# Performance work log

Hardware: AMD Instinct MI355X
Metric: run time of the kernel (lower is better)

Reference implementation:

```python
import jax, jax.numpy as jnp
from jax import lax
import numpy as np


def _dw_xcorr_single(f, k):
    # f: (ch, Hf, Wf) search features; k: (ch, Hk, Wk) template kernel
    # Depthwise cross-correlation: one 2D correlation per channel.
    ch = f.shape[0]
    out = lax.conv_general_dilated(
        f[None],                 # (1, ch, Hf, Wf)
        k[:, None],              # (ch, 1, Hk, Wk) OIHW depthwise kernel
        window_strides=(1, 1),
        padding='VALID',
        dimension_numbers=('NCHW', 'OIHW', 'NCHW'),
        feature_group_count=ch,
    )
    return out[0]  # (ch, H, W)


def _conv3x3(x, w, b):
    # x: (N, C, H, W), w: (O, C, 3, 3), b: (O,)
    y = lax.conv_general_dilated(
        x, w, window_strides=(1, 1), padding='VALID',
        dimension_numbers=('NCHW', 'OIHW', 'NCHW'))
    return y + b[None, :, None, None]


def setup_inputs() -> dict:
    key = jax.random.key(0)
    k1, k2, k3, k4, k5, k6 = jax.random.split(key, 6)
    N, C = 128, 256
    x_f = jax.random.normal(k1, (N, C, 31, 31), dtype=jnp.float32)
    z_f = jax.random.normal(k2, (N, C, 7, 7), dtype=jnp.float32)
    # Conv params (Kaiming-uniform-like scale)
    s3 = 1.0 / np.sqrt(C * 9)
    heat_w = jax.random.uniform(k3, (1, C, 3, 3), jnp.float32, -s3, s3)
    heat_b = jax.random.uniform(k4, (1,), jnp.float32, -s3, s3)
    reg_w = jax.random.uniform(k5, (4, C, 3, 3), jnp.float32, -s3, s3)
    reg_b = jax.random.uniform(k6, (4,), jnp.float32, -s3, s3)
    return {"x_f": x_f, "z_f": z_f, "heat_w": heat_w, "heat_b": heat_b,
            "reg_w": reg_w, "reg_b": reg_b}


def reference(x_f, z_f, heat_w, heat_b, reg_w, reg_b):
    # Depthwise cross-correlation over batch (groups = N*ch in the original)
    corr = jax.vmap(_dw_xcorr_single)(x_f, z_f)  # (N, C, 25, 25)
    pred_heat = _conv3x3(corr, heat_w, heat_b)   # (N, 1, 23, 23)
    pred_reg = _conv3x3(corr, reg_w, reg_b)      # (N, 4, 23, 23)
    return (pred_heat, pred_reg)
```

## Files before the change

### kernel.cpp

```cpp
#include <hip/hip_runtime.h>

#define NB 128
#define NC 256
#define HX 31
#define WX 31
#define HC 25
#define WC 25
#define HO 23
#define WO 23
#define CHUNKS 16
#define CPB (NC / CHUNKS)
#define GRP 8
#define ZCH 56
#define WCH 48
#define CCH (HC * WC)

#define NPIX (HO * WO)
#define HEAT_SZ (NB * NPIX)
#define REG_SZ  (NB * 4 * NPIX)
#define OUT_TOTAL (HEAT_SZ + REG_SZ)
#define NSTRIP3 (HO * 8)
#define PART_STRIDE (5 * NPIX)
#define WS_NEED ((size_t)NB * CHUNKS * PART_STRIDE * sizeof(float))

typedef float f4v __attribute__((ext_vector_type(4), aligned(4)));

__global__ void init_out_kernel(float* __restrict__ out,
                                const float* __restrict__ heat_b,
                                const float* __restrict__ reg_b) {
    int i = blockIdx.x * 256 + threadIdx.x;
    if (i >= OUT_TOTAL) return;
    if (i < HEAT_SZ) {
        out[i] = heat_b[0];
    } else {
        int j = i - HEAT_SZ;
        int o = (j / NPIX) & 3;
        out[i] = reg_b[o];
    }
}

__global__ void reduce_kernel(const float* __restrict__ part,
                              const float* __restrict__ heat_b,
                              const float* __restrict__ reg_b,
                              float* __restrict__ out) {
    int i = blockIdx.x * 256 + threadIdx.x;
    if (i >= OUT_TOTAL) return;
    int n, o, p;
    float b;
    if (i < HEAT_SZ) {
        n = i / NPIX; p = i - n * NPIX; o = 0; b = heat_b[0];
    } else {
        int j = i - HEAT_SZ;
        n = j / (4 * NPIX);
        int rm = j - n * 4 * NPIX;
        int r = rm / NPIX;
        p = rm - r * NPIX;
        o = 1 + r;
        b = reg_b[r];
    }
    const float* src = part + (size_t)n * CHUNKS * PART_STRIDE + o * NPIX + p;
    float s = b;
    #pragma unroll
    for (int c = 0; c < CHUNKS; ++c) s += src[(size_t)c * PART_STRIDE];
    out[i] = s;
}

template <bool USE_WS>
__launch_bounds__(256, 4)
__global__ void fused_head_kernel(const float* __restrict__ xf,
                                  const float* __restrict__ zf,
                                  const float* __restrict__ hw,
                                  const float* __restrict__ rw,
                                  float* __restrict__ out) {
    __shared__ __align__(16) float cs[GRP * CCH + 8];
    __shared__ __align__(16) float zs[GRP * ZCH];
    __shared__ __align__(16) float ws[CPB * WCH];

    const int tid = threadIdx.x;
    const int n = blockIdx.x >> 4;
    const int chunk = blockIdx.x & 15;
    const int cbase = chunk * CPB;

    const int cl = tid / 25;
    const int tt = tid % 25;
    const int tr = tt / 5, tc = tt % 5;
    const int i0 = tr * 5, j0 = tc * 5;

    const bool hasS = (tid < NSTRIP3);
    const int sy = tid >> 3;
    const int sx = tid & 7;
    const int cx = sx * 3;
    const int offS = sy * WC + cx;

    float accH[3] = {0.f, 0.f, 0.f};
    float accR[4][3] = {{0.f,0.f,0.f},{0.f,0.f,0.f},{0.f,0.f,0.f},{0.f,0.f,0.f}};

    const float* xn = xf + ((size_t)n * NC + cbase) * (HX * WX);
    const float* zn = zf + ((size_t)n * NC + cbase) * 49;

    for (int idx = tid; idx < CPB * 45; idx += 256) {
        int ch = idx / 45, j = idx - ch * 45;
        int c = cbase + ch;
        float v;
        if (j < 9) {
            v = hw[c * 9 + j];
        } else {
            int o = (j - 9) / 9;
            int jj = (j - 9) - o * 9;
            v = rw[((size_t)o * NC + c) * 9 + jj];
        }
        ws[ch * WCH + j] = v;
    }

    for (int g0 = 0; g0 < CPB; g0 += GRP) {
        for (int idx = tid; idx < GRP * 49; idx += 256) {
            int ch = idx / 49, q = idx - ch * 49;
            int u = q / 7, v = q - u * 7;
            zs[ch * ZCH + u * 8 + v] = zn[(size_t)(g0 + ch) * 49 + q];
        }
        __syncthreads();

        if (cl < GRP) {
            const float* xb = xn + (size_t)(g0 + cl) * (HX * WX) + i0 * WX + j0;
            const float* zb = zs + cl * ZCH;

            float cacc[5][5];
            #pragma unroll
            for (int r = 0; r < 5; ++r)
                #pragma unroll
                for (int b = 0; b < 5; ++b) cacc[r][b] = 0.f;

            f4v c0 = *(const f4v*)(xb);
            f4v c1 = *(const f4v*)(xb + 4);
            f4v c2 = *(const f4v*)(xb + 7);

            #pragma unroll
            for (int rl = 0; rl < 11; ++rl) {
                f4v n0, n1, n2;
                if (rl < 10) {
                    const float* rp = xb + (rl + 1) * WX;
                    n0 = *(const f4v*)(rp);
                    n1 = *(const f4v*)(rp + 4);
                    n2 = *(const f4v*)(rp + 7);
                }
                const float xr[11] = {c0.x, c0.y, c0.z, c0.w,
                                      c1.x, c1.y, c1.z, c1.w,
                                      c2.y, c2.z, c2.w};
                #pragma unroll
                for (int u = 0; u < 7; ++u) {
                    const int r = rl - u;
                    if (r >= 0 && r < 5) {
                        f4v za = *(const f4v*)(zb + u * 8);
                        f4v zc = *(const f4v*)(zb + u * 8 + 4);
                        const float zz[7] = {za.x, za.y, za.z, za.w,
                                             zc.x, zc.y, zc.z};
                        #pragma unroll
                        for (int v = 0; v < 7; ++v)
                            #pragma unroll
                            for (int b = 0; b < 5; ++b)
                                cacc[r][b] = fmaf(zz[v], xr[b + v], cacc[r][b]);
                    }
                }
                if (rl < 10) { c0 = n0; c1 = n1; c2 = n2; }
            }
            float* cb = cs + cl * CCH + i0 * WC + j0;
            #pragma unroll
            for (int r = 0; r < 5; ++r)
                #pragma unroll
                for (int b = 0; b < 5; ++b) cb[r * WC + b] = cacc[r][b];
        }
        __syncthreads();

        if (hasS) {
            for (int clc = 0; clc < GRP; ++clc) {
                float w[48];
                {
                    const f4v* wp = (const f4v*)(ws + (size_t)(g0 + clc) * WCH);
                    #pragma unroll
                    for (int q = 0; q < 12; ++q) {
                        f4v t = wp[q];
                        w[q * 4 + 0] = t.x; w[q * 4 + 1] = t.y;
                        w[q * 4 + 2] = t.z; w[q * 4 + 3] = t.w;
                    }
                }
                const float* base = cs + clc * CCH + offS;

                #pragma unroll
                for (int dy = 0; dy < 3; ++dy) {
                    f4v f = *(const f4v*)(base + dy * WC);
                    const float f4 = base[dy * WC + 4];
                    #pragma unroll
                    for (int dx = 0; dx < 3; ++dx) {
                        const int k = dy * 3 + dx;
                        #pragma unroll
                        for (int px = 0; px < 3; ++px) {
                            const int e = dx + px;
                            const float cv = (e < 4) ? f[e] : f4;
                            accH[px]    = fmaf(cv, w[k],      accH[px]);
                            accR[0][px] = fmaf(cv, w[9 + k],  accR[0][px]);
                            accR[1][px] = fmaf(cv, w[18 + k], accR[1][px]);
                            accR[2][px] = fmaf(cv, w[27 + k], accR[2][px]);
                            accR[3][px] = fmaf(cv, w[36 + k], accR[3][px]);
                        }
                    }
                }
            }
        }
        __syncthreads();
    }

    if (!hasS) return;
    const int p = sy * WO + cx;
    const bool full = (sx < 7);

    if (USE_WS) {
        float* part = out + (size_t)(n * CHUNKS + chunk) * PART_STRIDE;
        part[p + 0] = accH[0];
        part[p + 1] = accH[1];
        if (full) part[p + 2] = accH[2];
        #pragma unroll
        for (int o = 0; o < 4; ++o) {
            float* pr = part + (1 + o) * NPIX + p;
            pr[0] = accR[o][0];
            pr[1] = accR[o][1];
            if (full) pr[2] = accR[o][2];
        }
    } else {
        float* outH = out + n * NPIX + p;
        float* outR = out + HEAT_SZ + (size_t)n * 4 * NPIX + p;
        atomicAdd(&outH[0], accH[0]);
        atomicAdd(&outH[1], accH[1]);
        if (full) atomicAdd(&outH[2], accH[2]);
        #pragma unroll
        for (int o = 0; o < 4; ++o) {
            float* pr = outR + o * NPIX;
            atomicAdd(&pr[0], accR[o][0]);
            atomicAdd(&pr[1], accR[o][1]);
            if (full) atomicAdd(&pr[2], accR[o][2]);
        }
    }
}

extern "C" void kernel_launch(void* const* d_in, const int* in_sizes, int n_in,
                              void* d_out, int out_size, void* d_ws, size_t ws_size,
                              hipStream_t stream) {
    const float* x_f    = (const float*)d_in[0];
    const float* z_f    = (const float*)d_in[1];
    const float* heat_w = (const float*)d_in[2];
    const float* heat_b = (const float*)d_in[3];
    const float* reg_w  = (const float*)d_in[4];
    const float* reg_b  = (const float*)d_in[5];
    float* out = (float*)d_out;

    if (d_ws != nullptr && ws_size >= WS_NEED) {
        fused_head_kernel<true><<<NB * CHUNKS, 256, 0, stream>>>(
            x_f, z_f, heat_w, reg_w, (float*)d_ws);
        reduce_kernel<<<(OUT_TOTAL + 255) / 256, 256, 0, stream>>>(
            (const float*)d_ws, heat_b, reg_b, out);
    } else {
        init_out_kernel<<<(OUT_TOTAL + 255) / 256, 256, 0, stream>>>(out, heat_b, reg_b);
        fused_head_kernel<false><<<NB * CHUNKS, 256, 0, stream>>>(
            x_f, z_f, heat_w, reg_w, out);
    }
}
```

Before: 258.3 us.

## Stage search features in shared memory and halve channel group and chunk counts

Each group of channels now has its search-feature planes copied into shared memory with coalesced 16-byte loads, and the correlation loop reads rows from shared memory rather than making strided global loads per thread. GRP drops from 8 to 4 and CHUNKS from 16 to 8, so each block handles 32 channels in more, smaller groups, and there are half as many partial sums to reduce. Only 100 of 256 threads now do correlation work per group, and the larger shared footprint may reduce occupancy.

```diff
diff --git a/kernel.cpp b/kernel.cpp
--- a/kernel.cpp
+++ b/kernel.cpp
@@ -4,13 +4,14 @@
 #define NC 256
 #define HX 31
 #define WX 31
+#define XCH (HX * WX)
 #define HC 25
 #define WC 25
 #define HO 23
 #define WO 23
-#define CHUNKS 16
+#define CHUNKS 8
 #define CPB (NC / CHUNKS)
-#define GRP 8
+#define GRP 4
 #define ZCH 56
 #define WCH 48
 #define CCH (HC * WC)
@@ -72,13 +73,14 @@
                                   const float* __restrict__ hw,
                                   const float* __restrict__ rw,
                                   float* __restrict__ out) {
+    __shared__ __align__(16) float xs[GRP * XCH];
     __shared__ __align__(16) float cs[GRP * CCH + 8];
     __shared__ __align__(16) float zs[GRP * ZCH];
     __shared__ __align__(16) float ws[CPB * WCH];
 
     const int tid = threadIdx.x;
-    const int n = blockIdx.x >> 4;
-    const int chunk = blockIdx.x & 15;
+    const int n = blockIdx.x >> 3;
+    const int chunk = blockIdx.x & 7;
     const int cbase = chunk * CPB;
 
     const int cl = tid / 25;
@@ -95,7 +97,7 @@
     float accH[3] = {0.f, 0.f, 0.f};
     float accR[4][3] = {{0.f,0.f,0.f},{0.f,0.f,0.f},{0.f,0.f,0.f},{0.f,0.f,0.f}};
 
-    const float* xn = xf + ((size_t)n * NC + cbase) * (HX * WX);
+    const float* xn = xf + ((size_t)n * NC + cbase) * XCH;
     const float* zn = zf + ((size_t)n * NC + cbase) * 49;
 
     for (int idx = tid; idx < CPB * 45; idx += 256) {
@@ -113,15 +115,29 @@
     }
 
     for (int g0 = 0; g0 < CPB; g0 += GRP) {
-        for (int idx = tid; idx < GRP * 49; idx += 256) {
-            int ch = idx / 49, q = idx - ch * 49;
+        if (tid < GRP * 49) {
+            int ch = tid / 49, q = tid - ch * 49;
             int u = q / 7, v = q - u * 7;
             zs[ch * ZCH + u * 8 + v] = zn[(size_t)(g0 + ch) * 49 + q];
         }
+        {
+            const f4v* gx = (const f4v*)(xn + (size_t)g0 * XCH);
+            f4v* xs4 = (f4v*)xs;
+            const bool t3ok = (tid < 193);
+            f4v t0 = gx[tid];
+            f4v t1 = gx[tid + 256];
+            f4v t2 = gx[tid + 512];
+            f4v t3;
+            if (t3ok) t3 = gx[tid + 768];
+            xs4[tid]       = t0;
+            xs4[tid + 256] = t1;
+            xs4[tid + 512] = t2;
+            if (t3ok) xs4[tid + 768] = t3;
+        }
         __syncthreads();
 
         if (cl < GRP) {
-            const float* xb = xn + (size_t)(g0 + cl) * (HX * WX) + i0 * WX + j0;
+            const float* xb = xs + cl * XCH + i0 * WX + j0;
             const float* zb = zs + cl * ZCH;
 
             float cacc[5][5];
@@ -130,19 +146,12 @@
                 #pragma unroll
                 for (int b = 0; b < 5; ++b) cacc[r][b] = 0.f;
 
-            f4v c0 = *(const f4v*)(xb);
-            f4v c1 = *(const f4v*)(xb + 4);
-            f4v c2 = *(const f4v*)(xb + 7);
-
             #pragma unroll
             for (int rl = 0; rl < 11; ++rl) {
-                f4v n0, n1, n2;
-                if (rl < 10) {
-                    const float* rp = xb + (rl + 1) * WX;
-                    n0 = *(const f4v*)(rp);
-                    n1 = *(const f4v*)(rp + 4);
-                    n2 = *(const f4v*)(rp + 7);
-                }
+                const float* rp = xb + rl * WX;
+                f4v c0 = *(const f4v*)(rp);
+                f4v c1 = *(const f4v*)(rp + 4);
+                f4v c2 = *(const f4v*)(rp + 7);
                 const float xr[11] = {c0.x, c0.y, c0.z, c0.w,
                                       c1.x, c1.y, c1.z, c1.w,
                                       c2.y, c2.z, c2.w};
@@ -161,7 +170,6 @@
                                 cacc[r][b] = fmaf(zz[v], xr[b + v], cacc[r][b]);
                     }
                 }
-                if (rl < 10) { c0 = n0; c1 = n1; c2 = n2; }
             }
             float* cb = cs + cl * CCH + i0 * WC + j0;
             #pragma unroll
```

Result: slower. 269.4 us (+4.3%).

## Halve channel chunks, widen groups, double-buffer template loads, use atomics

Applied to the files above, without the earlier changes.

The channel split per sample drops from 16 to 8 chunks, and each group now holds 10 channels instead of 8, with a remainder group for the last channels. Template (z) loads for the next group are prefetched into registers and written to a second shared buffer, which overlaps global latency with the 3x3 conv stage and removes one barrier per group. The workspace partial-sum plus reduce-kernel path is dropped in favour of an init kernel and atomicAdd accumulation. In exchange there are fewer blocks (1024), more LDS per block, and a possibly nondeterministic summation order.

```diff
diff --git a/kernel.cpp b/kernel.cpp
--- a/kernel.cpp
+++ b/kernel.cpp
@@ -8,9 +8,9 @@
 #define WC 25
 #define HO 23
 #define WO 23
-#define CHUNKS 16
+#define CHUNKS 8
 #define CPB (NC / CHUNKS)
-#define GRP 8
+#define GRP 10
 #define ZCH 56
 #define WCH 48
 #define CCH (HC * WC)
@@ -20,8 +20,6 @@
 #define REG_SZ  (NB * 4 * NPIX)
 #define OUT_TOTAL (HEAT_SZ + REG_SZ)
 #define NSTRIP3 (HO * 8)
-#define PART_STRIDE (5 * NPIX)
-#define WS_NEED ((size_t)NB * CHUNKS * PART_STRIDE * sizeof(float))
 
 typedef float f4v __attribute__((ext_vector_type(4), aligned(4)));
 
@@ -39,33 +37,6 @@
     }
 }
 
-__global__ void reduce_kernel(const float* __restrict__ part,
-                              const float* __restrict__ heat_b,
-                              const float* __restrict__ reg_b,
-                              float* __restrict__ out) {
-    int i = blockIdx.x * 256 + threadIdx.x;
-    if (i >= OUT_TOTAL) return;
-    int n, o, p;
-    float b;
-    if (i < HEAT_SZ) {
-        n = i / NPIX; p = i - n * NPIX; o = 0; b = heat_b[0];
-    } else {
-        int j = i - HEAT_SZ;
-        n = j / (4 * NPIX);
-        int rm = j - n * 4 * NPIX;
-        int r = rm / NPIX;
-        p = rm - r * NPIX;
-        o = 1 + r;
-        b = reg_b[r];
-    }
-    const float* src = part + (size_t)n * CHUNKS * PART_STRIDE + o * NPIX + p;
-    float s = b;
-    #pragma unroll
-    for (int c = 0; c < CHUNKS; ++c) s += src[(size_t)c * PART_STRIDE];
-    out[i] = s;
-}
-
-template <bool USE_WS>
 __launch_bounds__(256, 4)
 __global__ void fused_head_kernel(const float* __restrict__ xf,
                                   const float* __restrict__ zf,
@@ -73,12 +44,12 @@
                                   const float* __restrict__ rw,
                                   float* __restrict__ out) {
     __shared__ __align__(16) float cs[GRP * CCH + 8];
-    __shared__ __align__(16) float zs[GRP * ZCH];
+    __shared__ __align__(16) float zs[2][GRP * ZCH];
     __shared__ __align__(16) float ws[CPB * WCH];
 
     const int tid = threadIdx.x;
-    const int n = blockIdx.x >> 4;
-    const int chunk = blockIdx.x & 15;
+    const int n = blockIdx.x >> 3;
+    const int chunk = blockIdx.x & 7;
     const int cbase = chunk * CPB;
 
     const int cl = tid / 25;
@@ -112,17 +83,21 @@
         ws[ch * WCH + j] = v;
     }
 
-    for (int g0 = 0; g0 < CPB; g0 += GRP) {
-        for (int idx = tid; idx < GRP * 49; idx += 256) {
-            int ch = idx / 49, q = idx - ch * 49;
-            int u = q / 7, v = q - u * 7;
-            zs[ch * ZCH + u * 8 + v] = zn[(size_t)(g0 + ch) * 49 + q];
-        }
-        __syncthreads();
-
-        if (cl < GRP) {
+    for (int idx = tid; idx < GRP * 49; idx += 256) {
+        int ch = idx / 49, q = idx - ch * 49;
+        int u = q / 7, v = q - u * 7;
+        zs[0][ch * ZCH + u * 8 + v] = zn[idx];
+    }
+    __syncthreads();
+
+    int gi = 0;
+    for (int g0 = 0; g0 < CPB; g0 += GRP, ++gi) {
+        const int G = (CPB - g0) < GRP ? (CPB - g0) : GRP;
+        const float* zsb = zs[gi & 1];
+
+        if (cl < G) {
             const float* xb = xn + (size_t)(g0 + cl) * (HX * WX) + i0 * WX + j0;
-            const float* zb = zs + cl * ZCH;
+            const float* zb = zsb + cl * ZCH;
 
             float cacc[5][5];
             #pragma unroll
@@ -169,10 +144,18 @@
                 #pragma unroll
                 for (int b = 0; b < 5; ++b) cb[r * WC + b] = cacc[r][b];
         }
+
+        const int g1 = g0 + GRP;
+        const bool pf = (g1 < CPB);
+        const int cnt = pf ? ((CPB - g1) < GRP ? (CPB - g1) : GRP) * 49 : 0;
+        float zr0 = 0.f, zr1 = 0.f;
+        if (tid < cnt)       zr0 = zn[(size_t)g1 * 49 + tid];
+        if (tid + 256 < cnt) zr1 = zn[(size_t)g1 * 49 + tid + 256];
+
         __syncthreads();
 
         if (hasS) {
-            for (int clc = 0; clc < GRP; ++clc) {
+            for (int clc = 0; clc < G; ++clc) {
                 float w[48];
                 {
                     const f4v* wp = (const f4v*)(ws + (size_t)(g0 + clc) * WCH);
@@ -206,6 +189,19 @@
                 }
             }
         }
+
+        if (tid < cnt) {
+            int ch = tid / 49, q = tid - ch * 49;
+            int u = q / 7, v = q - u * 7;
+            zs[(gi + 1) & 1][ch * ZCH + u * 8 + v] = zr0;
+        }
+        if (tid + 256 < cnt) {
+            int q2 = tid + 256;
+            int ch = q2 / 49, q = q2 - ch * 49;
+            int u = q / 7, v = q - u * 7;
+            zs[(gi + 1) & 1][ch * ZCH + u * 8 + v] = zr1;
+        }
+
         __syncthreads();
     }
 
@@ -213,31 +209,17 @@
     const int p = sy * WO + cx;
     const bool full = (sx < 7);
 
-    if (USE_WS) {
-        float* part = out + (size_t)(n * CHUNKS + chunk) * PART_STRIDE;
-        part[p + 0] = accH[0];
-        part[p + 1] = accH[1];
-        if (full) part[p + 2] = accH[2];
-        #pragma unroll
-        for (int o = 0; o < 4; ++o) {
-            float* pr = part + (1 + o) * NPIX + p;
-            pr[0] = accR[o][0];
-            pr[1] = accR[o][1];
-            if (full) pr[2] = accR[o][2];
-        }
-    } else {
-        float* outH = out + n * NPIX + p;
-        float* outR = out + HEAT_SZ + (size_t)n * 4 * NPIX + p;
-        atomicAdd(&outH[0], accH[0]);
-        atomicAdd(&outH[1], accH[1]);
-        if (full) atomicAdd(&outH[2], accH[2]);
-        #pragma unroll
-        for (int o = 0; o < 4; ++o) {
-            float* pr = outR + o * NPIX;
-            atomicAdd(&pr[0], accR[o][0]);
-            atomicAdd(&pr[1], accR[o][1]);
-            if (full) atomicAdd(&pr[2], accR[o][2]);
-        }
+    float* outH = out + n * NPIX + p;
+    float* outR = out + HEAT_SZ + (size_t)n * 4 * NPIX + p;
+    atomicAdd(&outH[0], accH[0]);
+    atomicAdd(&outH[1], accH[1]);
+    if (full) atomicAdd(&outH[2], accH[2]);
+    #pragma unroll
+    for (int o = 0; o < 4; ++o) {
+        float* pr = outR + o * NPIX;
+        atomicAdd(&pr[0], accR[o][0]);
+        atomicAdd(&pr[1], accR[o][1]);
+        if (full) atomicAdd(&pr[2], accR[o][2]);
     }
 }
 
@@ -252,14 +234,6 @@
     const float* reg_b  = (const float*)d_in[5];
     float* out = (float*)d_out;
 
-    if (d_ws != nullptr && ws_size >= WS_NEED) {
-        fused_head_kernel<true><<<NB * CHUNKS, 256, 0, stream>>>(
-            x_f, z_f, heat_w, reg_w, (float*)d_ws);
-        reduce_kernel<<<(OUT_TOTAL + 255) / 256, 256, 0, stream>>>(
-            (const float*)d_ws, heat_b, reg_b, out);
-    } else {
-        init_out_kernel<<<(OUT_TOTAL + 255) / 256, 256, 0, stream>>>(out, heat_b, reg_b);
-        fused_head_kernel<false><<<NB * CHUNKS, 256, 0, stream>>>(
-            x_f, z_f, heat_w, reg_w, out);
-    }
+    init_out_kernel<<<(OUT_TOTAL + 255) / 256, 256, 0, stream>>>(out, heat_b, reg_b);
+    fused_head_kernel<<<NB * CHUNKS, 256, 0, stream>>>(x_f, z_f, heat_w, reg_w, out);
 }
```

Result: slower. 294.7 us (+14.1%).
